# Kernel optimization log

Measured on AMD Instinct MI355X. Metric: run time of the kernel, lower is better.

Reference implementation:

```python
import jax, jax.numpy as jnp
import numpy as np

SHAPE = (128, 128, 128)  # (D, H, W), batch_size = 1
N = 100000               # number of active voxels
CONV_CH = [(3, 64), (64, 64), (64, 96), (96, 96), (96, 128), (128, 128),
           (128, 160), (160, 160), (160, 192), (192, 192), (192, 224),
           (224, 224), (224, 256), (256, 256)]


def _lin(c, shape):
    Sz, Sy, Sx = shape
    return ((c[:, 0] * Sz + c[:, 1]) * Sy + c[:, 2]) * Sx + c[:, 3]


def _subm_pairs(coords, shape):
    # Submanifold conv indice pairs: for each active voxel and each of the
    # 27 kernel offsets, the row index of the active neighbor, or -1.
    Sz, Sy, Sx = shape
    n = coords.shape[0]
    grid = np.full(Sz * Sy * Sx, -1, np.int64)  # batch size 1 dense lookup (like self.grid)
    grid[_lin(coords, shape)] = np.arange(n)
    pairs = []
    for dz in (-1, 0, 1):
        for dy in (-1, 0, 1):
            for dx in (-1, 0, 1):
                z = coords[:, 1] + dz
                y = coords[:, 2] + dy
                x = coords[:, 3] + dx
                ok = (z >= 0) & (z < Sz) & (y >= 0) & (y < Sy) & (x >= 0) & (x < Sx)
                nl = ((coords[:, 0] * Sz + z) * Sy + y) * Sx + x
                pairs.append(np.where(ok, grid[np.clip(nl, 0, grid.size - 1)], -1))
    return np.stack(pairs)  # [27, n]


def _pool_structure(coords, shape):
    # SparseMaxPool3d(2,2): output sites = unique coords//2; inv maps each
    # input voxel to its output window.
    ns = tuple(s // 2 for s in shape)
    c2 = coords.copy()
    c2[:, 1:] = c2[:, 1:] // 2
    key = _lin(c2, ns)
    uniq, inv = np.unique(key, return_inverse=True)
    Sz, Sy, Sx = ns
    b = uniq // (Sz * Sy * Sx)
    r = uniq % (Sz * Sy * Sx)
    z = r // (Sy * Sx)
    r = r % (Sy * Sx)
    nc = np.stack([b, z, r // Sx, r % Sx], 1).astype(np.int64)
    return nc, inv, uniq.shape[0], ns


def _build_plan(coors_np):
    # Paired SubMConv3d layers share an indice_key -> same pairs per level.
    coords = coors_np.astype(np.int64)
    shape = SHAPE
    plan = []
    for lvl in range(7):
        p = jnp.asarray(_subm_pairs(coords, shape))
        plan.append(('conv', p))
        plan.append(('conv', p))
        if lvl < 6:
            coords, inv, m, shape = _pool_structure(coords, shape)
            plan.append(('pool', jnp.asarray(inv), m))
    return plan


def _subm_conv(feats, pairs, W):
    # gather -> GEMM -> accumulate, per kernel offset (W: [27, Cin, Cout])
    out = jnp.zeros((feats.shape[0], W.shape[2]), feats.dtype)
    for k in range(27):
        idx = pairs[k]
        g = jnp.where((idx >= 0)[:, None], feats[jnp.clip(idx, 0)], 0.0)
        out = out + g @ W[k]
    return out


def _forward(feats, weights, plan):
    wi = 0
    for step in plan:
        if step[0] == 'conv':
            feats = _subm_conv(feats, step[1], weights[wi])
            wi += 1
        else:
            feats = jax.ops.segment_max(feats, step[1], num_segments=step[2])
    return feats


def setup_inputs() -> dict:
    rng = np.random.default_rng(0)
    lin = rng.choice(SHAPE[0] * SHAPE[1] * SHAPE[2], size=N, replace=False)
    z = lin // (SHAPE[1] * SHAPE[2])
    r = lin % (SHAPE[1] * SHAPE[2])
    coors = np.stack([np.zeros(N, np.int32), z.astype(np.int32),
                      (r // SHAPE[2]).astype(np.int32), (r % SHAPE[2]).astype(np.int32)], 1)
    key = jax.random.key(0)
    keys = jax.random.split(key, len(CONV_CH) + 1)
    inp = {
        'features': jax.random.normal(keys[0], (N, 3), jnp.float32),
        'coors': jnp.asarray(coors),
        'batch_size': 1,
    }
    for i, (ci, co) in enumerate(CONV_CH):
        inp[f'w{i}'] = jax.random.normal(keys[i + 1], (27, ci, co), jnp.float32) * (1.0 / np.sqrt(27.0 * ci))
    return inp


def reference(features, coors, batch_size, w0, w1, w2, w3, w4, w5, w6, w7, w8, w9, w10, w11, w12, w13):
    plan = _build_plan(np.asarray(coors))
    ws = [w0, w1, w2, w3, w4, w5, w6, w7, w8, w9, w10, w11, w12, w13]
    return _forward(features, ws, plan)
```

## Files before the change

### kernel.cpp

```cpp
#include <hip/hip_runtime.h>
#include <cstdint>
#include <cstddef>


typedef __attribute__((ext_vector_type(8))) short short8v;
typedef __attribute__((ext_vector_type(4))) float f32x4;

static inline int cdiv_h(int a, int b) { return (a + b - 1) / b; }

__device__ inline unsigned short f2bf(float f) {
    unsigned int u = __builtin_bit_cast(unsigned int, f);
    u += 0x7FFFu + ((u >> 16) & 1u);
    return (unsigned short)(u >> 16);
}
__device__ inline float bf2f(unsigned short h) {
    unsigned int u = ((unsigned int)h) << 16;
    return __builtin_bit_cast(float, u);
}

__device__ inline void gload_lds16(const void* g, void* l) {
    auto gp = (const __attribute__((address_space(1))) unsigned int*)(uintptr_t)g;
    auto lp = (__attribute__((address_space(3))) unsigned int*)(uintptr_t)l;
    __builtin_amdgcn_global_load_lds(gp, lp, 16, 0, 0);
}

__global__ void set_count_k(int* counts, int n) { counts[0] = n; }

__global__ void scatter_grid_k(const int* __restrict__ coords, const int* __restrict__ cnt,
                               int* __restrict__ grid, int S)
{
    int i = blockIdx.x * blockDim.x + threadIdx.x;
    if (i >= cnt[0]) return;
    int z = coords[i * 4 + 1], y = coords[i * 4 + 2], x = coords[i * 4 + 3];
    grid[(z * S + y) * S + x] = i;
}

__global__ void build_pairs_k(const int* __restrict__ coords, const int* __restrict__ cnt,
                              const int* __restrict__ grid, int* __restrict__ pairs_t, int S)
{
    int i = blockIdx.x * blockDim.x + threadIdx.x;
    if (i >= cnt[0]) return;
    int z = coords[i * 4 + 1], y = coords[i * 4 + 2], x = coords[i * 4 + 3];
    int4* dst = reinterpret_cast<int4*>(pairs_t + (size_t)i * 32);
#pragma unroll
    for (int g = 0; g < 7; ++g) {
        int4 q;
#pragma unroll
        for (int j = 0; j < 4; ++j) {
            int k = g * 4 + j;
            int v = -1;
            if (k < 27) {
                int nz = z + k / 9 - 1;
                int ny = y + (k / 3) % 3 - 1;
                int nx = x + k % 3 - 1;
                if (nz >= 0 && nz < S && ny >= 0 && ny < S && nx >= 0 && nx < S)
                    v = grid[(nz * S + ny) * S + nx];
            }
            ((int*)&q)[j] = v;
        }
        dst[g] = q;
    }
}

struct PackArgs {
    const float* src[13];
    unsigned short* dst[13];
    int cin[13];
    int cout[13];
    int tileStart[14];
};

__global__ __launch_bounds__(256) void pack_all_k(PackArgs pa)
{
    int g = blockIdx.x * 4 + ((int)threadIdx.x >> 6);
    int lane = (int)threadIdx.x & 63;
    if (g >= pa.tileStart[13]) return;
    int li = 0;
    while (li < 12 && g >= pa.tileStart[li + 1]) ++li;
    int tile = g - pa.tileStart[li];
    int CIN = pa.cin[li], COUT = pa.cout[li];
    int NS = CIN >> 5, NT = COUT >> 4;
    int t = tile % NT;
    int s = (tile / NT) % NS;
    int k = tile / (NT * NS);
    int kabs = s * 32 + (lane >> 4) * 8;
    int c = t * 16 + (lane & 15);
    const float* src = pa.src[li] + ((size_t)(k * CIN + kabs)) * COUT + c;
    unsigned short* dst = pa.dst[li] + (size_t)tile * 512 + lane * 8;
#pragma unroll
    for (int j = 0; j < 8; ++j) dst[j] = f2bf(src[(size_t)j * COUT]);
}

__global__ __launch_bounds__(256) void conv0_k(
    const float* __restrict__ fin, const float* __restrict__ W,
    const int* __restrict__ pairs_t, const int* __restrict__ cnt,
    unsigned short* __restrict__ fout)
{
    const int row = blockIdx.x * 16 + ((int)threadIdx.x >> 4);
    const int cg = ((int)threadIdx.x & 15) * 4;
    if (row >= cnt[0]) return;
    float a0 = 0, a1 = 0, a2 = 0, a3 = 0;
    for (int k = 0; k < 27; ++k) {
        int nb = pairs_t[(size_t)row * 32 + k];
        if (nb < 0) continue;
        const float* fr = fin + (size_t)nb * 3;
        const float* wk = W + (size_t)k * 3 * 64 + cg;
#pragma unroll
        for (int ci = 0; ci < 3; ++ci) {
            float f = fr[ci];
            float4 w = *reinterpret_cast<const float4*>(wk + ci * 64);
            a0 += f * w.x; a1 += f * w.y; a2 += f * w.z; a3 += f * w.w;
        }
    }
    size_t o = (size_t)row * 64 + cg;
    fout[o] = f2bf(a0); fout[o + 1] = f2bf(a1);
    fout[o + 2] = f2bf(a2); fout[o + 3] = f2bf(a3);
}

template <int CIN, int COUT, int RT, bool OUTF32>
__global__ __launch_bounds__(256) void conv_lds_k(
    const unsigned short* __restrict__ fin, const unsigned short* __restrict__ Wp,
    const int* __restrict__ pairs_t, const int* __restrict__ cnt,
    void* __restrict__ fout)
{
    constexpr int NS = CIN / 32, NT = COUT / 16;
    constexpr int NCH = NS * NT;
    __shared__ unsigned short sB[2][NCH * 512];

    const int lane = (int)threadIdx.x & 63;
    const int wave = (int)threadIdx.x >> 6;
    const int l15 = lane & 15, lhi = lane >> 4;
    const int M = cnt[0];
    const int rowBase = (blockIdx.x * 4 + wave) * (RT * 16);

    const unsigned short* __restrict__ finL = fin + (size_t)lhi * 8;

    f32x4 acc[RT][NT];
#pragma unroll
    for (int a = 0; a < RT; ++a)
#pragma unroll
        for (int b = 0; b < NT; ++b) acc[a][b] = (f32x4){0.f, 0.f, 0.f, 0.f};

    int  rowC[RT];
    bool rOK[RT];
#pragma unroll
    for (int rt = 0; rt < RT; ++rt) {
        int r = rowBase + rt * 16 + l15;
        rOK[rt]  = r < M;
        rowC[rt] = rOK[rt] ? r : 0;
    }

#define STAGE(K, BUF)                                                            \
    {                                                                            \
        const unsigned short* src =                                              \
            Wp + (size_t)(K) * (NCH * 512) + (size_t)lane * 8;                   \
        _Pragma("unroll") for (int idx = wave; idx < NCH; idx += 4)              \
            gload_lds16(src + (size_t)idx * 512, &sB[BUF][idx * 512]);           \
    }

    int nbCur[RT], nbNxt[RT];
#pragma unroll
    for (int rt = 0; rt < RT; ++rt)
        nbCur[rt] = rOK[rt] ? pairs_t[(size_t)rowC[rt] * 32 + 0] : -1;

    STAGE(0, 0);

    for (int k = 0; k < 27; ++k) {
        __syncthreads();
        if (k < 26) {
            STAGE(k + 1, (k + 1) & 1);
#pragma unroll
            for (int rt = 0; rt < RT; ++rt)
                nbNxt[rt] = rOK[rt] ? pairs_t[(size_t)rowC[rt] * 32 + (k + 1)] : -1;
        }

        int nb[RT], act[RT];
        bool anyAct = false;
#pragma unroll
        for (int rt = 0; rt < RT; ++rt) {
            nb[rt] = nbCur[rt];
            act[rt] = __any(nb[rt] >= 0);
            anyAct = anyAct || (act[rt] != 0);
        }
#pragma unroll
        for (int rt = 0; rt < RT; ++rt) nbCur[rt] = nbNxt[rt];

        if (anyAct) {
            const unsigned short* __restrict__ buf = sB[k & 1];
            short8v afr[NS][RT];
#pragma unroll
            for (int s = 0; s < NS; ++s)
#pragma unroll
                for (int rt = 0; rt < RT; ++rt) {
                    afr[s][rt] = (short8v){};
                    if (nb[rt] >= 0)
                        afr[s][rt] = *reinterpret_cast<const short8v*>(
                            finL + (size_t)nb[rt] * CIN + s * 32);
                }
#pragma unroll
            for (int s = 0; s < NS; ++s)
#pragma unroll
                for (int rt = 0; rt < RT; ++rt) {
                    if (!act[rt]) continue;
#pragma unroll
                    for (int t = 0; t < NT; ++t) {
                        short8v b = *reinterpret_cast<const short8v*>(
                            &buf[(s * NT + t) * 512 + lane * 8]);
                        acc[rt][t] = __builtin_amdgcn_mfma_f32_16x16x32_bf16(
                            afr[s][rt], b, acc[rt][t], 0, 0, 0);
                    }
                }
        }
    }
#undef STAGE

#pragma unroll
    for (int rt = 0; rt < RT; ++rt) {
#pragma unroll
        for (int j = 0; j < 4; ++j) {
            int r = rowBase + rt * 16 + lhi * 4 + j;
            if (r >= M) continue;
#pragma unroll
            for (int t = 0; t < NT; ++t) {
                int c = t * 16 + l15;
                if constexpr (OUTF32)
                    ((float*)fout)[(size_t)r * COUT + c] = acc[rt][t][j];
                else
                    ((unsigned short*)fout)[(size_t)r * COUT + c] = f2bf(acc[rt][t][j]);
            }
        }
    }
}

template <int CIN, int COUT, int CTD, int TG>
__global__ __launch_bounds__(64) void conv_deep_k(
    const unsigned short* __restrict__ fin, const unsigned short* __restrict__ Wp,
    const int* __restrict__ pairs_t, const int* __restrict__ cnt,
    float* __restrict__ fout)
{
    constexpr int NS = CIN / 32, NT = COUT / 16;
    const int lane = (int)threadIdx.x;
    const int l15 = lane & 15, lhi = lane >> 4;
    const int M = cnt[0];
    if ((int)blockIdx.x * 16 >= M) return;
    const int row = blockIdx.x * 16 + l15;
    const int ct0 = blockIdx.y * CTD;
    const int k0 = blockIdx.z * TG;

    f32x4 acc[CTD];
#pragma unroll
    for (int t = 0; t < CTD; ++t) acc[t] = (f32x4){0.f, 0.f, 0.f, 0.f};

    bool anyTap = false;
#pragma unroll
    for (int kk = 0; kk < TG; ++kk) {
        const int k = k0 + kk;
        int nb = (row < M) ? pairs_t[(size_t)row * 32 + k] : -1;
        if (!__any(nb >= 0)) continue;
        anyTap = true;
        const unsigned short* wk = Wp + (size_t)k * NS * NT * 512 + (size_t)lane * 8;
#pragma unroll
        for (int s = 0; s < NS; ++s) {
            short8v a = (short8v){};
            if (nb >= 0)
                a = *reinterpret_cast<const short8v*>(
                    fin + (size_t)nb * CIN + s * 32 + lhi * 8);
#pragma unroll
            for (int t = 0; t < CTD; ++t) {
                short8v b = *reinterpret_cast<const short8v*>(
                    wk + ((size_t)s * NT + ct0 + t) * 512);
                acc[t] = __builtin_amdgcn_mfma_f32_16x16x32_bf16(a, b, acc[t], 0, 0, 0);
            }
        }
    }
    if (!anyTap) return;

#pragma unroll
    for (int t = 0; t < CTD; ++t)
#pragma unroll
        for (int j = 0; j < 4; ++j) {
            int r = blockIdx.x * 16 + lhi * 4 + j;
            if (r < M)
                atomicAdd(&fout[(size_t)r * COUT + (ct0 + t) * 16 + l15], acc[t][j]);
        }
}

__global__ __launch_bounds__(256) void f32_to_bf16_k(
    const float* __restrict__ src, const int* __restrict__ cnt,
    unsigned short* __restrict__ dst, int C)
{
    int idx = blockIdx.x * 256 + (int)threadIdx.x;
    if (idx / C >= cnt[0]) return;
    dst[idx] = f2bf(src[idx]);
}

__global__ void mark_occ_k(const int* __restrict__ coords, const int* __restrict__ cnt,
                           int* __restrict__ occ, int Sh)
{
    int i = blockIdx.x * blockDim.x + threadIdx.x;
    if (i >= cnt[0]) return;
    int z = coords[i * 4 + 1] >> 1, y = coords[i * 4 + 2] >> 1, x = coords[i * 4 + 3] >> 1;
    occ[(z * Sh + y) * Sh + x] = 1;
}

__global__ __launch_bounds__(256) void scan_sum_k(const int* __restrict__ occ, int P,
                                                  int* __restrict__ bsum)
{
    int base = blockIdx.x * 4096 + (int)threadIdx.x * 16;
    int s = 0;
#pragma unroll
    for (int j = 0; j < 16; ++j) { int i = base + j; s += (i < P) ? occ[i] : 0; }
    for (int off = 1; off < 64; off <<= 1) s += __shfl_xor(s, off);
    __shared__ int ws[4];
    if ((threadIdx.x & 63) == 0) ws[threadIdx.x >> 6] = s;
    __syncthreads();
    if (threadIdx.x == 0) bsum[blockIdx.x] = ws[0] + ws[1] + ws[2] + ws[3];
}

__global__ void scan_offsets_k(const int* __restrict__ bsum, int nb,
                               int* __restrict__ boff, int* __restrict__ cntOut)
{
    int lane = threadIdx.x;
    int v = (lane < nb) ? bsum[lane] : 0;
    int incl = v;
    for (int off = 1; off < 64; off <<= 1) {
        int t = __shfl_up(incl, off);
        if (lane >= off) incl += t;
    }
    if (lane < nb) boff[lane] = incl - v;
    if (lane == 63) cntOut[0] = incl;
}

__global__ __launch_bounds__(256) void scan_emit_k(const int* __restrict__ occ, int P,
                                                   const int* __restrict__ boff,
                                                   int* __restrict__ newcoords, int Sh)
{
    __shared__ int ws[4];
    int tid = threadIdx.x;
    int base = blockIdx.x * 4096 + tid * 16;
    int v[16];
    int s = 0;
#pragma unroll
    for (int j = 0; j < 16; ++j) { int i = base + j; v[j] = (i < P) ? occ[i] : 0; s += v[j]; }
    int mysum = s;
    int incl = s;
    for (int off = 1; off < 64; off <<= 1) {
        int t = __shfl_up(incl, off);
        if ((tid & 63) >= off) incl += t;
    }
    if ((tid & 63) == 63) ws[tid >> 6] = incl;
    __syncthreads();
    int waveOff = 0;
    for (int w = 0; w < (tid >> 6); ++w) waveOff += ws[w];
    int r = boff[blockIdx.x] + waveOff + incl - mysum;
    const int SS = Sh * Sh;
#pragma unroll
    for (int j = 0; j < 16; ++j) {
        if (v[j]) {
            int c = base + j;
            newcoords[r * 4 + 0] = 0;
            newcoords[r * 4 + 1] = c / SS;
            newcoords[r * 4 + 2] = (c % SS) / Sh;
            newcoords[r * 4 + 3] = c % Sh;
            ++r;
        }
    }
}

__global__ void pool_max_k(const unsigned short* __restrict__ fin, const int* __restrict__ gridPrev,
                           const int* __restrict__ newcoords, const int* __restrict__ cnt,
                           unsigned short* __restrict__ fout, int C, int Sprev)
{
    int idx = blockIdx.x * blockDim.x + threadIdx.x;
    int r = idx / C, c = idx % C;
    if (r >= cnt[0]) return;
    int z2 = newcoords[r * 4 + 1] * 2;
    int y2 = newcoords[r * 4 + 2] * 2;
    int x2 = newcoords[r * 4 + 3] * 2;
    float best = -3.4e38f;
    unsigned short bb = 0;
#pragma unroll
    for (int d = 0; d < 8; ++d) {
        int z = z2 + (d >> 2), y = y2 + ((d >> 1) & 1), x = x2 + (d & 1);
        int j = gridPrev[(z * Sprev + y) * Sprev + x];
        if (j >= 0) {
            unsigned short u = fin[(size_t)j * C + c];
            float f = bf2f(u);
            if (f > best) { best = f; bb = u; }
        }
    }
    fout[(size_t)r * C + c] = bb;
}


template <int CIN, int COUT, int RT, bool OUTF32>
static void launch_cl(const unsigned short* fin, const unsigned short* Wp,
                      const int* pairs_t, const int* cnt, void* fout,
                      int bound, hipStream_t stream)
{
    static_assert(CIN % 32 == 0 && COUT % 16 == 0, "shape");
    dim3 g(cdiv_h(bound, RT * 64));
    conv_lds_k<CIN, COUT, RT, OUTF32><<<g, 256, 0, stream>>>(fin, Wp, pairs_t, cnt, fout);
}

template <int CIN, int COUT, int CTD, int TG>
static void launch_deep(const unsigned short* fin, const unsigned short* Wp,
                        const int* pairs_t, const int* cnt, float* acc,
                        int bound, hipStream_t stream)
{
    constexpr int NT = COUT / 16;
    static_assert(NT % CTD == 0 && 27 % TG == 0, "shape");
    dim3 g(cdiv_h(bound, 16), NT / CTD, 27 / TG);
    conv_deep_k<CIN, COUT, CTD, TG><<<g, 64, 0, stream>>>(fin, Wp, pairs_t, cnt, acc);
}

extern "C" void kernel_launch(void* const* d_in, const int* in_sizes, int n_in,
                              void* d_out, int out_size, void* d_ws, size_t ws_size,
                              hipStream_t stream)
{
    const float* feats0 = (const float*)d_in[0];
    const int*   coors  = (const int*)d_in[1];
    const float* w[14];
    for (int i = 0; i < 14; ++i) w[i] = (const float*)d_in[3 + i];
    float* out = (float*)d_out;
    const int N = in_sizes[0] / 3;

    char* p = (char*)d_ws;
    int* grid   = (int*)p; p += (size_t)128 * 128 * 128 * 4;
    int* occ    = (int*)p; p += (size_t)64 * 64 * 64 * 4;
    int* counts = (int*)p; p += 256;
    int* bsum   = (int*)p; p += 256;
    int* boff   = (int*)p; p += 256;
    int* pairs_t = (int*)p; p += (size_t)N * 32 * 4;
    int* coordsA = (int*)p; p += (size_t)N * 16;
    int* coordsB = (int*)p; p += (size_t)N * 16;
    unsigned short* featA = (unsigned short*)p; p += (size_t)N * 96 * 2;
    unsigned short* featB = (unsigned short*)p; p += (size_t)N * 96 * 2;
    float* scratch = (float*)p; p += (size_t)4096 * 160 * 4 + 1024;
    unsigned short* wpBase = (unsigned short*)p;

    static const int CH[14][2] = {{3,64},{64,64},{64,96},{96,96},{96,128},{128,128},
                                  {128,160},{160,160},{160,192},{192,192},{192,224},
                                  {224,224},{224,256},{256,256}};
    unsigned short* wp[14];
    PackArgs pa;
    {
        size_t off = 0;
        int ts = 0;
        for (int i = 1; i < 14; ++i) {
            wp[i] = wpBase + off;
            off += (size_t)27 * CH[i][0] * CH[i][1];
            pa.src[i - 1] = w[i];
            pa.dst[i - 1] = wp[i];
            pa.cin[i - 1] = CH[i][0];
            pa.cout[i - 1] = CH[i][1];
            pa.tileStart[i - 1] = ts;
            ts += 27 * (CH[i][0] / 32) * (CH[i][1] / 16);
        }
        pa.tileStart[13] = ts;
    }

    int bounds[7];
    for (int l = 0; l < 7; ++l) {
        int S = 128 >> l, c = S * S * S;
        bounds[l] = N < c ? N : c;
    }

    set_count_k<<<1, 1, 0, stream>>>(counts, N);
    hipMemsetAsync(d_out, 0, (size_t)out_size * 4, stream);
    pack_all_k<<<cdiv_h(pa.tileStart[13], 4), 256, 0, stream>>>(pa);

    auto build_level = [&](const int* coordsL, int lvl) {
        int S = 128 >> lvl;
        hipMemsetAsync(grid, 0xFF, (size_t)S * S * S * 4, stream);
        int blocks = cdiv_h(bounds[lvl], 256);
        scatter_grid_k<<<blocks, 256, 0, stream>>>(coordsL, counts + lvl, grid, S);
        build_pairs_k<<<blocks, 256, 0, stream>>>(coordsL, counts + lvl, grid, pairs_t, S);
    };

    auto do_pool = [&](const int* coordsL, int lvl, const unsigned short* fin,
                       unsigned short* fout, int C, int* coordsOut) {
        int S = 128 >> lvl, Sh = S / 2, P = Sh * Sh * Sh;
        hipMemsetAsync(occ, 0, (size_t)P * 4, stream);
        mark_occ_k<<<cdiv_h(bounds[lvl], 256), 256, 0, stream>>>(coordsL, counts + lvl, occ, Sh);
        int nb = cdiv_h(P, 4096);
        scan_sum_k<<<nb, 256, 0, stream>>>(occ, P, bsum);
        scan_offsets_k<<<1, 64, 0, stream>>>(bsum, nb, boff, counts + lvl + 1);
        scan_emit_k<<<nb, 256, 0, stream>>>(occ, P, boff, coordsOut, Sh);
        int total = bounds[lvl + 1] * C;
        pool_max_k<<<cdiv_h(total, 256), 256, 0, stream>>>(fin, grid, coordsOut,
                                                           counts + lvl + 1, fout, C, S);
    };

    auto deep_conv = [&](auto launcher, const unsigned short* fin, int wi, int lvl,
                         unsigned short* dst, int COUT) {
        hipMemsetAsync(scratch, 0, (size_t)bounds[lvl] * COUT * 4, stream);
        launcher(fin, wp[wi], pairs_t, counts + lvl, scratch, bounds[lvl], stream);
        f32_to_bf16_k<<<cdiv_h(bounds[lvl] * COUT, 256), 256, 0, stream>>>(
            scratch, counts + lvl, dst, COUT);
    };

    build_level(coors, 0);
    conv0_k<<<cdiv_h(bounds[0], 16), 256, 0, stream>>>(feats0, w[0], pairs_t, counts + 0, featA);
    launch_cl<64, 64, 2, false>(featA, wp[1], pairs_t, counts + 0, featB, bounds[0], stream);
    do_pool(coors, 0, featB, featA, 64, coordsA);
    build_level(coordsA, 1);
    launch_cl<64, 96, 2, false>(featA, wp[2], pairs_t, counts + 1, featB, bounds[1], stream);
    launch_cl<96, 96, 2, false>(featB, wp[3], pairs_t, counts + 1, featA, bounds[1], stream);
    do_pool(coordsA, 1, featA, featB, 96, coordsB);
    build_level(coordsB, 2);
    launch_cl<96, 128, 2, false>(featB, wp[4], pairs_t, counts + 2, featA, bounds[2], stream);
    launch_cl<128, 128, 2, false>(featA, wp[5], pairs_t, counts + 2, featB, bounds[2], stream);
    do_pool(coordsB, 2, featB, featA, 128, coordsA);
    build_level(coordsA, 3);
    deep_conv(launch_deep<128, 160, 2, 3>, featA, 6, 3, featB, 160);
    deep_conv(launch_deep<160, 160, 2, 3>, featB, 7, 3, featA, 160);
    do_pool(coordsA, 3, featA, featB, 160, coordsB);
    build_level(coordsB, 4);
    deep_conv(launch_deep<160, 192, 2, 3>, featB, 8, 4, featA, 192);
    deep_conv(launch_deep<192, 192, 2, 3>, featA, 9, 4, featB, 192);
    do_pool(coordsB, 4, featB, featA, 192, coordsA);
    build_level(coordsA, 5);
    deep_conv(launch_deep<192, 224, 1, 1>, featA, 10, 5, featB, 224);
    deep_conv(launch_deep<224, 224, 1, 1>, featB, 11, 5, featA, 224);
    do_pool(coordsA, 5, featA, featB, 224, coordsB);
    build_level(coordsB, 6);
    deep_conv(launch_deep<224, 256, 1, 1>, featB, 12, 6, featA, 256);
    launch_deep<256, 256, 1, 1>(featA, wp[13], pairs_t, counts + 6, out, bounds[6], stream);
}
```

Baseline: 745.0 us.

## Split LDS conv over output-channel tiles and fuse f32-to-bf16 into consumers

The LDS conv kernel gains a second grid dimension over output-channel tiles (CT). Each block stages only its slice of the weights and hoists the B-fragment loads out of the row loop, which raises parallelism and cuts LDS footprint. The deep conv and pool kernels now read the f32 atomic scratch directly and convert to bf16 inline, so the separate f32_to_bf16 kernels disappear and two scratch buffers alternate. The trade-off is that gathered f32 input reads are twice as wide, and feature gathers for the LDS convs are repeated once per channel tile.

```diff
diff --git a/kernel.cpp b/kernel.cpp
--- a/kernel.cpp
+++ b/kernel.cpp
@@ -117,14 +117,14 @@
     fout[o + 2] = f2bf(a2); fout[o + 3] = f2bf(a3);
 }
 
-template <int CIN, int COUT, int RT, bool OUTF32>
+template <int CIN, int COUT, int RT, int CT, bool OUTF32>
 __global__ __launch_bounds__(256) void conv_lds_k(
     const unsigned short* __restrict__ fin, const unsigned short* __restrict__ Wp,
     const int* __restrict__ pairs_t, const int* __restrict__ cnt,
     void* __restrict__ fout)
 {
     constexpr int NS = CIN / 32, NT = COUT / 16;
-    constexpr int NCH = NS * NT;
+    constexpr int NCH = NS * CT;
     __shared__ unsigned short sB[2][NCH * 512];
 
     const int lane = (int)threadIdx.x & 63;
@@ -132,14 +132,15 @@
     const int l15 = lane & 15, lhi = lane >> 4;
     const int M = cnt[0];
     const int rowBase = (blockIdx.x * 4 + wave) * (RT * 16);
+    const int ct0 = blockIdx.y * CT;
 
     const unsigned short* __restrict__ finL = fin + (size_t)lhi * 8;
 
-    f32x4 acc[RT][NT];
+    f32x4 acc[RT][CT];
 #pragma unroll
     for (int a = 0; a < RT; ++a)
 #pragma unroll
-        for (int b = 0; b < NT; ++b) acc[a][b] = (f32x4){0.f, 0.f, 0.f, 0.f};
+        for (int b = 0; b < CT; ++b) acc[a][b] = (f32x4){0.f, 0.f, 0.f, 0.f};
 
     int  rowC[RT];
     bool rOK[RT];
@@ -150,12 +151,18 @@
         rowC[rt] = rOK[rt] ? r : 0;
     }
 
-#define STAGE(K, BUF)                                                            \
-    {                                                                            \
-        const unsigned short* src =                                              \
-            Wp + (size_t)(K) * (NCH * 512) + (size_t)lane * 8;                   \
-        _Pragma("unroll") for (int idx = wave; idx < NCH; idx += 4)              \
-            gload_lds16(src + (size_t)idx * 512, &sB[BUF][idx * 512]);           \
+#define STAGE(K, BUF)                                                              \
+    {                                                                              \
+        const unsigned short* srcB = Wp + (size_t)(K) * (NS * NT * 512)            \
+                                     + (size_t)lane * 8;                           \
+        _Pragma("unroll") for (int ii = 0; ii < (NCH + 3) / 4; ++ii) {             \
+            int idx = wave + ii * 4;                                               \
+            if (idx < NCH) {                                                       \
+                int s = idx / CT, tt = idx % CT;                                   \
+                gload_lds16(srcB + ((size_t)s * NT + ct0 + tt) * 512,              \
+                            &sB[BUF][idx * 512]);                                  \
+            }                                                                      \
+        }                                                                          \
     }
 
     int nbCur[RT], nbNxt[RT];
@@ -198,18 +205,21 @@
                             finL + (size_t)nb[rt] * CIN + s * 32);
                 }
 #pragma unroll
-            for (int s = 0; s < NS; ++s)
+            for (int s = 0; s < NS; ++s) {
+                short8v bb[CT];
+#pragma unroll
+                for (int t = 0; t < CT; ++t)
+                    bb[t] = *reinterpret_cast<const short8v*>(
+                        &buf[(s * CT + t) * 512 + lane * 8]);
 #pragma unroll
                 for (int rt = 0; rt < RT; ++rt) {
                     if (!act[rt]) continue;
 #pragma unroll
-                    for (int t = 0; t < NT; ++t) {
-                        short8v b = *reinterpret_cast<const short8v*>(
-                            &buf[(s * NT + t) * 512 + lane * 8]);
+                    for (int t = 0; t < CT; ++t)
                         acc[rt][t] = __builtin_amdgcn_mfma_f32_16x16x32_bf16(
-                            afr[s][rt], b, acc[rt][t], 0, 0, 0);
-                    }
+                            afr[s][rt], bb[t], acc[rt][t], 0, 0, 0);
                 }
+            }
         }
     }
 #undef STAGE
@@ -221,8 +231,8 @@
             int r = rowBase + rt * 16 + lhi * 4 + j;
             if (r >= M) continue;
 #pragma unroll
-            for (int t = 0; t < NT; ++t) {
-                int c = t * 16 + l15;
+            for (int t = 0; t < CT; ++t) {
+                int c = (ct0 + t) * 16 + l15;
                 if constexpr (OUTF32)
                     ((float*)fout)[(size_t)r * COUT + c] = acc[rt][t][j];
                 else
@@ -232,9 +242,9 @@
     }
 }
 
-template <int CIN, int COUT, int CTD, int TG>
+template <int CIN, int COUT, int CTD, int TG, bool INF32>
 __global__ __launch_bounds__(64) void conv_deep_k(
-    const unsigned short* __restrict__ fin, const unsigned short* __restrict__ Wp,
+    const void* __restrict__ fin, const unsigned short* __restrict__ Wp,
     const int* __restrict__ pairs_t, const int* __restrict__ cnt,
     float* __restrict__ fout)
 {
@@ -262,9 +272,17 @@
 #pragma unroll
         for (int s = 0; s < NS; ++s) {
             short8v a = (short8v){};
-            if (nb >= 0)
-                a = *reinterpret_cast<const short8v*>(
-                    fin + (size_t)nb * CIN + s * 32 + lhi * 8);
+            if (nb >= 0) {
+                if constexpr (INF32) {
+                    const float* fr = (const float*)fin + (size_t)nb * CIN + s * 32 + lhi * 8;
+#pragma unroll
+                    for (int j = 0; j < 8; ++j)
+                        ((unsigned short*)&a)[j] = f2bf(fr[j]);
+                } else {
+                    a = *reinterpret_cast<const short8v*>(
+                        (const unsigned short*)fin + (size_t)nb * CIN + s * 32 + lhi * 8);
+                }
+            }
 #pragma unroll
             for (int t = 0; t < CTD; ++t) {
                 short8v b = *reinterpret_cast<const short8v*>(
@@ -283,15 +301,6 @@
             if (r < M)
                 atomicAdd(&fout[(size_t)r * COUT + (ct0 + t) * 16 + l15], acc[t][j]);
         }
-}
-
-__global__ __launch_bounds__(256) void f32_to_bf16_k(
-    const float* __restrict__ src, const int* __restrict__ cnt,
-    unsigned short* __restrict__ dst, int C)
-{
-    int idx = blockIdx.x * 256 + (int)threadIdx.x;
-    if (idx / C >= cnt[0]) return;
-    dst[idx] = f2bf(src[idx]);
 }
 
 __global__ void mark_occ_k(const int* __restrict__ coords, const int* __restrict__ cnt,
@@ -367,7 +376,8 @@
     }
 }
 
-__global__ void pool_max_k(const unsigned short* __restrict__ fin, const int* __restrict__ gridPrev,
+template <bool INF32>
+__global__ void pool_max_k(const void* __restrict__ fin, const int* __restrict__ gridPrev,
                            const int* __restrict__ newcoords, const int* __restrict__ cnt,
                            unsigned short* __restrict__ fout, int C, int Sprev)
 {
@@ -384,34 +394,40 @@
         int z = z2 + (d >> 2), y = y2 + ((d >> 1) & 1), x = x2 + (d & 1);
         int j = gridPrev[(z * Sprev + y) * Sprev + x];
         if (j >= 0) {
-            unsigned short u = fin[(size_t)j * C + c];
-            float f = bf2f(u);
-            if (f > best) { best = f; bb = u; }
-        }
-    }
-    fout[(size_t)r * C + c] = bb;
-}
-
-
-template <int CIN, int COUT, int RT, bool OUTF32>
+            if constexpr (INF32) {
+                float f = ((const float*)fin)[(size_t)j * C + c];
+                if (f > best) best = f;
+            } else {
+                unsigned short u = ((const unsigned short*)fin)[(size_t)j * C + c];
+                float f = bf2f(u);
+                if (f > best) { best = f; bb = u; }
+            }
+        }
+    }
+    fout[(size_t)r * C + c] = INF32 ? f2bf(best) : bb;
+}
+
+
+template <int CIN, int COUT, int RT, int CT, bool OUTF32>
 static void launch_cl(const unsigned short* fin, const unsigned short* Wp,
                       const int* pairs_t, const int* cnt, void* fout,
                       int bound, hipStream_t stream)
 {
-    static_assert(CIN % 32 == 0 && COUT % 16 == 0, "shape");
-    dim3 g(cdiv_h(bound, RT * 64));
-    conv_lds_k<CIN, COUT, RT, OUTF32><<<g, 256, 0, stream>>>(fin, Wp, pairs_t, cnt, fout);
-}
-
-template <int CIN, int COUT, int CTD, int TG>
-static void launch_deep(const unsigned short* fin, const unsigned short* Wp,
+    constexpr int NT = COUT / 16;
+    static_assert(CIN % 32 == 0 && COUT % 16 == 0 && NT % CT == 0, "shape");
+    dim3 g(cdiv_h(bound, RT * 64), NT / CT);
+    conv_lds_k<CIN, COUT, RT, CT, OUTF32><<<g, 256, 0, stream>>>(fin, Wp, pairs_t, cnt, fout);
+}
+
+template <int CIN, int COUT, int CTD, int TG, bool INF32>
+static void launch_deep(const void* fin, const unsigned short* Wp,
                         const int* pairs_t, const int* cnt, float* acc,
                         int bound, hipStream_t stream)
 {
     constexpr int NT = COUT / 16;
     static_assert(NT % CTD == 0 && 27 % TG == 0, "shape");
     dim3 g(cdiv_h(bound, 16), NT / CTD, 27 / TG);
-    conv_deep_k<CIN, COUT, CTD, TG><<<g, 64, 0, stream>>>(fin, Wp, pairs_t, cnt, acc);
+    conv_deep_k<CIN, COUT, CTD, TG, INF32><<<g, 64, 0, stream>>>(fin, Wp, pairs_t, cnt, acc);
 }
 
 extern "C" void kernel_launch(void* const* d_in, const int* in_sizes, int n_in,
@@ -436,7 +452,8 @@
     int* coordsB = (int*)p; p += (size_t)N * 16;
     unsigned short* featA = (unsigned short*)p; p += (size_t)N * 96 * 2;
     unsigned short* featB = (unsigned short*)p; p += (size_t)N * 96 * 2;
-    float* scratch = (float*)p; p += (size_t)4096 * 160 * 4 + 1024;
+    float* scrA = (float*)p; p += (size_t)4096 * 192 * 4;
+    float* scrB = (float*)p; p += (size_t)4096 * 192 * 4;
     unsigned short* wpBase = (unsigned short*)p;
 
     static const int CH[14][2] = {{3,64},{64,64},{64,96},{96,96},{96,128},{128,128},
@@ -478,7 +495,7 @@
         build_pairs_k<<<blocks, 256, 0, stream>>>(coordsL, counts + lvl, grid, pairs_t, S);
     };
 
-    auto do_pool = [&](const int* coordsL, int lvl, const unsigned short* fin,
+    auto do_pool = [&](const int* coordsL, int lvl, const void* fin, bool inF32,
                        unsigned short* fout, int C, int* coordsOut) {
         int S = 128 >> lvl, Sh = S / 2, P = Sh * Sh * Sh;
         hipMemsetAsync(occ, 0, (size_t)P * 4, stream);
@@ -488,43 +505,46 @@
         scan_offsets_k<<<1, 64, 0, stream>>>(bsum, nb, boff, counts + lvl + 1);
         scan_emit_k<<<nb, 256, 0, stream>>>(occ, P, boff, coordsOut, Sh);
         int total = bounds[lvl + 1] * C;
-        pool_max_k<<<cdiv_h(total, 256), 256, 0, stream>>>(fin, grid, coordsOut,
-                                                           counts + lvl + 1, fout, C, S);
-    };
-
-    auto deep_conv = [&](auto launcher, const unsigned short* fin, int wi, int lvl,
-                         unsigned short* dst, int COUT) {
-        hipMemsetAsync(scratch, 0, (size_t)bounds[lvl] * COUT * 4, stream);
-        launcher(fin, wp[wi], pairs_t, counts + lvl, scratch, bounds[lvl], stream);
-        f32_to_bf16_k<<<cdiv_h(bounds[lvl] * COUT, 256), 256, 0, stream>>>(
-            scratch, counts + lvl, dst, COUT);
+        if (inF32)
+            pool_max_k<true><<<cdiv_h(total, 256), 256, 0, stream>>>(
+                fin, grid, coordsOut, counts + lvl + 1, fout, C, S);
+        else
+            pool_max_k<false><<<cdiv_h(total, 256), 256, 0, stream>>>(
+                fin, grid, coordsOut, counts + lvl + 1, fout, C, S);
     };
 
     build_level(coors, 0);
     conv0_k<<<cdiv_h(bounds[0], 16), 256, 0, stream>>>(feats0, w[0], pairs_t, counts + 0, featA);
-    launch_cl<64, 64, 2, false>(featA, wp[1], pairs_t, counts + 0, featB, bounds[0], stream);
-    do_pool(coors, 0, featB, featA, 64, coordsA);
+    launch_cl<64, 64, 2, 4, false>(featA, wp[1], pairs_t, counts + 0, featB, bounds[0], stream);
+    do_pool(coors, 0, featB, false, featA, 64, coordsA);
     build_level(coordsA, 1);
-    launch_cl<64, 96, 2, false>(featA, wp[2], pairs_t, counts + 1, featB, bounds[1], stream);
-    launch_cl<96, 96, 2, false>(featB, wp[3], pairs_t, counts + 1, featA, bounds[1], stream);
-    do_pool(coordsA, 1, featA, featB, 96, coordsB);
+    launch_cl<64, 96, 2, 3, false>(featA, wp[2], pairs_t, counts + 1, featB, bounds[1], stream);
+    launch_cl<96, 96, 2, 3, false>(featB, wp[3], pairs_t, counts + 1, featA, bounds[1], stream);
+    do_pool(coordsA, 1, featA, false, featB, 96, coordsB);
     build_level(coordsB, 2);
-    launch_cl<96, 128, 2, false>(featB, wp[4], pairs_t, counts + 2, featA, bounds[2], stream);
-    launch_cl<128, 128, 2, false>(featA, wp[5], pairs_t, counts + 2, featB, bounds[2], stream);
-    do_pool(coordsB, 2, featB, featA, 128, coordsA);
+    launch_cl<96, 128, 2, 4, false>(featB, wp[4], pairs_t, counts + 2, featA, bounds[2], stream);
+    launch_cl<128, 128, 2, 4, false>(featA, wp[5], pairs_t, counts + 2, featB, bounds[2], stream);
+    do_pool(coordsB, 2, featB, false, featA, 128, coordsA);
     build_level(coordsA, 3);
-    deep_conv(launch_deep<128, 160, 2, 3>, featA, 6, 3, featB, 160);
-    deep_conv(launch_deep<160, 160, 2, 3>, featB, 7, 3, featA, 160);
-    do_pool(coordsA, 3, featA, featB, 160, coordsB);
+    hipMemsetAsync(scrA, 0, (size_t)bounds[3] * 160 * 4, stream);
+    launch_deep<128, 160, 2, 3, false>(featA, wp[6], pairs_t, counts + 3, scrA, bounds[3], stream);
+    hipMemsetAsync(scrB, 0, (size_t)bounds[3] * 160 * 4, stream);
+    launch_deep<160, 160, 2, 3, true>(scrA, wp[7], pairs_t, counts + 3, scrB, bounds[3], stream);
+    do_pool(coordsA, 3, scrB, true, featB, 160, coordsB);
     build_level(coordsB, 4);
-    deep_conv(launch_deep<160, 192, 2, 3>, featB, 8, 4, featA, 192);
-    deep_conv(launch_deep<192, 192, 2, 3>, featA, 9, 4, featB, 192);
-    do_pool(coordsB, 4, featB, featA, 192, coordsA);
+    hipMemsetAsync(scrA, 0, (size_t)bounds[4] * 192 * 4, stream);
+    launch_deep<160, 192, 2, 3, false>(featB, wp[8], pairs_t, counts + 4, scrA, bounds[4], stream);
+    hipMemsetAsync(scrB, 0, (size_t)bounds[4] * 192 * 4, stream);
+    launch_deep<192, 192, 2, 3, true>(scrA, wp[9], pairs_t, counts + 4, scrB, bounds[4], stream);
+    do_pool(coordsB, 4, scrB, true, featA, 192, coordsA);
     build_level(coordsA, 5);
-    deep_conv(launch_deep<192, 224, 1, 1>, featA, 10, 5, featB, 224);
-    deep_conv(launch_deep<224, 224, 1, 1>, featB, 11, 5, featA, 224);
-    do_pool(coordsA, 5, featA, featB, 224, coordsB);
+    hipMemsetAsync(scrA, 0, (size_t)bounds[5] * 224 * 4, stream);
+    launch_deep<192, 224, 1, 1, false>(featA, wp[10], pairs_t, counts + 5, scrA, bounds[5], stream);
+    hipMemsetAsync(scrB, 0, (size_t)bounds[5] * 224 * 4, stream);
+    launch_deep<224, 224, 1, 1, true>(scrA, wp[11], pairs_t, counts + 5, scrB, bounds[5], stream);
+    do_pool(coordsA, 5, scrB, true, featB, 224, coordsB);
     build_level(coordsB, 6);
-    deep_conv(launch_deep<224, 256, 1, 1>, featB, 12, 6, featA, 256);
-    launch_deep<256, 256, 1, 1>(featA, wp[13], pairs_t, counts + 6, out, bounds[6], stream);
-}
+    hipMemsetAsync(scrA, 0, (size_t)bounds[6] * 256 * 4, stream);
+    launch_deep<224, 256, 1, 1, false>(featB, wp[12], pairs_t, counts + 6, scrA, bounds[6], stream);
+    launch_deep<256, 256, 1, 1, true>(scrA, wp[13], pairs_t, counts + 6, out, bounds[6], stream);
+}
```

Result: slower. 814.7 us (+9.4%).

## Split output channels across blocks in LDS conv and swizzle block IDs per XCD

Applied to the files above, without the earlier changes.

Adds CT/GY template parameters so the LDS conv kernel can split the output-channel tiles across GY blocks, each staging only its slice of the weights into LDS. This is used for the level-2 convs (GY=2). It also remaps block IDs with an XCD-aware swizzle so neighbouring logical blocks land on the same XCD, and hoists B-fragment LDS reads out of the row-tile loop. The aim is more blocks and less LDS per block on the small level-2 grids, at the cost of re-gathering input rows once per channel split. The scratch buffer size also changes.

```diff
diff --git a/kernel.cpp b/kernel.cpp
--- a/kernel.cpp
+++ b/kernel.cpp
@@ -22,6 +22,12 @@
     auto gp = (const __attribute__((address_space(1))) unsigned int*)(uintptr_t)g;
     auto lp = (__attribute__((address_space(3))) unsigned int*)(uintptr_t)l;
     __builtin_amdgcn_global_load_lds(gp, lp, 16, 0, 0);
+}
+
+__device__ inline int xcd_swz(int bid, int nwg) {
+    int q = nwg >> 3, r = nwg & 7;
+    int x = bid & 7, idx = bid >> 3;
+    return (x < r ? x * (q + 1) : r * (q + 1) + (x - r) * q) + idx;
 }
 
 __global__ void set_count_k(int* counts, int n) { counts[0] = n; }
@@ -117,29 +123,33 @@
     fout[o + 2] = f2bf(a2); fout[o + 3] = f2bf(a3);
 }
 
-template <int CIN, int COUT, int RT, bool OUTF32>
+template <int CIN, int COUT, int RT, int CT, int GY, bool OUTF32>
 __global__ __launch_bounds__(256) void conv_lds_k(
     const unsigned short* __restrict__ fin, const unsigned short* __restrict__ Wp,
     const int* __restrict__ pairs_t, const int* __restrict__ cnt,
     void* __restrict__ fout)
 {
     constexpr int NS = CIN / 32, NT = COUT / 16;
-    constexpr int NCH = NS * NT;
+    constexpr int NCH = NS * CT;
     __shared__ unsigned short sB[2][NCH * 512];
 
     const int lane = (int)threadIdx.x & 63;
     const int wave = (int)threadIdx.x >> 6;
     const int l15 = lane & 15, lhi = lane >> 4;
     const int M = cnt[0];
-    const int rowBase = (blockIdx.x * 4 + wave) * (RT * 16);
+
+    const int lid = xcd_swz((int)blockIdx.x, (int)gridDim.x);
+    const int rowBlock = lid / GY;
+    const int ct0 = (lid % GY) * CT;
+    const int rowBase = (rowBlock * 4 + wave) * (RT * 16);
 
     const unsigned short* __restrict__ finL = fin + (size_t)lhi * 8;
 
-    f32x4 acc[RT][NT];
+    f32x4 acc[RT][CT];
 #pragma unroll
     for (int a = 0; a < RT; ++a)
 #pragma unroll
-        for (int b = 0; b < NT; ++b) acc[a][b] = (f32x4){0.f, 0.f, 0.f, 0.f};
+        for (int b = 0; b < CT; ++b) acc[a][b] = (f32x4){0.f, 0.f, 0.f, 0.f};
 
     int  rowC[RT];
     bool rOK[RT];
@@ -150,12 +160,18 @@
         rowC[rt] = rOK[rt] ? r : 0;
     }
 
-#define STAGE(K, BUF)                                                            \
-    {                                                                            \
-        const unsigned short* src =                                              \
-            Wp + (size_t)(K) * (NCH * 512) + (size_t)lane * 8;                   \
-        _Pragma("unroll") for (int idx = wave; idx < NCH; idx += 4)              \
-            gload_lds16(src + (size_t)idx * 512, &sB[BUF][idx * 512]);           \
+#define STAGE(K, BUF)                                                              \
+    {                                                                              \
+        const unsigned short* srcB = Wp + (size_t)(K) * (NS * NT * 512)            \
+                                     + (size_t)lane * 8;                           \
+        _Pragma("unroll") for (int ii = 0; ii < (NCH + 3) / 4; ++ii) {             \
+            int idx = wave + ii * 4;                                               \
+            if (idx < NCH) {                                                       \
+                int s = idx / CT, tt = idx % CT;                                   \
+                gload_lds16(srcB + ((size_t)s * NT + ct0 + tt) * 512,              \
+                            &sB[BUF][idx * 512]);                                  \
+            }                                                                      \
+        }                                                                          \
     }
 
     int nbCur[RT], nbNxt[RT];
@@ -198,18 +214,21 @@
                             finL + (size_t)nb[rt] * CIN + s * 32);
                 }
 #pragma unroll
-            for (int s = 0; s < NS; ++s)
+            for (int s = 0; s < NS; ++s) {
+                short8v bb[CT];
+#pragma unroll
+                for (int t = 0; t < CT; ++t)
+                    bb[t] = *reinterpret_cast<const short8v*>(
+                        &buf[(s * CT + t) * 512 + lane * 8]);
 #pragma unroll
                 for (int rt = 0; rt < RT; ++rt) {
                     if (!act[rt]) continue;
 #pragma unroll
-                    for (int t = 0; t < NT; ++t) {
-                        short8v b = *reinterpret_cast<const short8v*>(
-                            &buf[(s * NT + t) * 512 + lane * 8]);
+                    for (int t = 0; t < CT; ++t)
                         acc[rt][t] = __builtin_amdgcn_mfma_f32_16x16x32_bf16(
-                            afr[s][rt], b, acc[rt][t], 0, 0, 0);
-                    }
+                            afr[s][rt], bb[t], acc[rt][t], 0, 0, 0);
                 }
+            }
         }
     }
 #undef STAGE
@@ -221,8 +240,8 @@
             int r = rowBase + rt * 16 + lhi * 4 + j;
             if (r >= M) continue;
 #pragma unroll
-            for (int t = 0; t < NT; ++t) {
-                int c = t * 16 + l15;
+            for (int t = 0; t < CT; ++t) {
+                int c = (ct0 + t) * 16 + l15;
                 if constexpr (OUTF32)
                     ((float*)fout)[(size_t)r * COUT + c] = acc[rt][t][j];
                 else
@@ -393,14 +412,16 @@
 }
 
 
-template <int CIN, int COUT, int RT, bool OUTF32>
+template <int CIN, int COUT, int RT, int CT, int GY, bool OUTF32>
 static void launch_cl(const unsigned short* fin, const unsigned short* Wp,
                       const int* pairs_t, const int* cnt, void* fout,
                       int bound, hipStream_t stream)
 {
-    static_assert(CIN % 32 == 0 && COUT % 16 == 0, "shape");
-    dim3 g(cdiv_h(bound, RT * 64));
-    conv_lds_k<CIN, COUT, RT, OUTF32><<<g, 256, 0, stream>>>(fin, Wp, pairs_t, cnt, fout);
+    constexpr int NT = COUT / 16;
+    static_assert(CIN % 32 == 0 && COUT % 16 == 0 && CT * GY == NT, "shape");
+    dim3 g(cdiv_h(bound, RT * 64) * GY);
+    conv_lds_k<CIN, COUT, RT, CT, GY, OUTF32><<<g, 256, 0, stream>>>(fin, Wp, pairs_t,
+                                                                     cnt, fout);
 }
 
 template <int CIN, int COUT, int CTD, int TG>
@@ -436,7 +457,7 @@
     int* coordsB = (int*)p; p += (size_t)N * 16;
     unsigned short* featA = (unsigned short*)p; p += (size_t)N * 96 * 2;
     unsigned short* featB = (unsigned short*)p; p += (size_t)N * 96 * 2;
-    float* scratch = (float*)p; p += (size_t)4096 * 160 * 4 + 1024;
+    float* scratch = (float*)p; p += (size_t)4096 * 192 * 4;
     unsigned short* wpBase = (unsigned short*)p;
 
     static const int CH[14][2] = {{3,64},{64,64},{64,96},{96,96},{96,128},{128,128},
@@ -502,15 +523,15 @@
 
     build_level(coors, 0);
     conv0_k<<<cdiv_h(bounds[0], 16), 256, 0, stream>>>(feats0, w[0], pairs_t, counts + 0, featA);
-    launch_cl<64, 64, 2, false>(featA, wp[1], pairs_t, counts + 0, featB, bounds[0], stream);
+    launch_cl<64, 64, 2, 4, 1, false>(featA, wp[1], pairs_t, counts + 0, featB, bounds[0], stream);
     do_pool(coors, 0, featB, featA, 64, coordsA);
     build_level(coordsA, 1);
-    launch_cl<64, 96, 2, false>(featA, wp[2], pairs_t, counts + 1, featB, bounds[1], stream);
-    launch_cl<96, 96, 2, false>(featB, wp[3], pairs_t, counts + 1, featA, bounds[1], stream);
+    launch_cl<64, 96, 2, 6, 1, false>(featA, wp[2], pairs_t, counts + 1, featB, bounds[1], stream);
+    launch_cl<96, 96, 2, 6, 1, false>(featB, wp[3], pairs_t, counts + 1, featA, bounds[1], stream);
     do_pool(coordsA, 1, featA, featB, 96, coordsB);
     build_level(coordsB, 2);
-    launch_cl<96, 128, 2, false>(featB, wp[4], pairs_t, counts + 2, featA, bounds[2], stream);
-    launch_cl<128, 128, 2, false>(featA, wp[5], pairs_t, counts + 2, featB, bounds[2], stream);
+    launch_cl<96, 128, 2, 4, 2, false>(featB, wp[4], pairs_t, counts + 2, featA, bounds[2], stream);
+    launch_cl<128, 128, 2, 4, 2, false>(featA, wp[5], pairs_t, counts + 2, featB, bounds[2], stream);
     do_pool(coordsB, 2, featB, featA, 128, coordsA);
     build_level(coordsA, 3);
     deep_conv(launch_deep<128, 160, 2, 3>, featA, 6, 3, featB, 160);
```

Measured after the change: 746.5 us. Within noise of the previous version (+0.2%).
